# Kernel tuning notes

Measured on AMD Instinct MI355X. Metric: run time of the kernel, lower is better.

## Reference

```python
import jax, jax.numpy as jnp
import numpy as np

D_MODEL = 1024
N_HEAD = 16
DK = D_MODEL // N_HEAD
NEG = -10000.0  # module uses masked_fill with -10000.0, not -inf


def setup_inputs() -> dict:
    key = jax.random.key(0)
    k1, k2, k3 = jax.random.split(key, 3)
    B, T = 8, 1024
    x = jax.random.normal(k1, (B, T, D_MODEL), dtype=jnp.float32)
    # torch Linear(d, 3d, bias=False): y = x @ W.T with W [3d, d]; store transposed
    w_qkv = jax.random.normal(k2, (D_MODEL, 3 * D_MODEL), dtype=jnp.float32) * (1.0 / np.sqrt(D_MODEL))
    w_proj = jax.random.normal(k3, (D_MODEL, D_MODEL), dtype=jnp.float32) * (1.0 / np.sqrt(D_MODEL))
    return {"x": x, "w_qkv": w_qkv, "w_proj": w_proj}


def reference(x, w_qkv, w_proj):
    B, T, C = x.shape
    qkv = x @ w_qkv  # [B, T, 3C]
    q, k, v = jnp.split(qkv, 3, axis=-1)
    # [B, H, T, dk]
    q = q.reshape(B, T, N_HEAD, DK).transpose(0, 2, 1, 3)
    k = k.reshape(B, T, N_HEAD, DK).transpose(0, 2, 1, 3)
    v = v.reshape(B, T, N_HEAD, DK).transpose(0, 2, 1, 3)
    att = jnp.einsum('bhqd,bhkd->bhqk', q, k) / jnp.sqrt(jnp.float32(DK))
    causal = jnp.tril(jnp.ones((T, T), dtype=bool))  # [T, T]
    att = jnp.where(causal[None, None], att, NEG)
    att = jax.nn.softmax(att, axis=-1)
    y = jnp.einsum('bhqk,bhkd->bhqd', att, v)  # [B, H, T, dk]
    y = y.transpose(0, 2, 1, 3).reshape(B, T, C)
    return y @ w_proj
```

## Files before the change

kernel.cpp:

```cpp
#include <hip/hip_runtime.h>

typedef short bf16x8 __attribute__((ext_vector_type(8)));
typedef float f32x4 __attribute__((ext_vector_type(4)));

__device__ __forceinline__ unsigned short f2bf(float f) {
  unsigned u = __builtin_bit_cast(unsigned, f);
  u += 0x7fff + ((u >> 16) & 1);
  return (unsigned short)(u >> 16);
}

__device__ __forceinline__ void gload_lds16(const void* g, void* l) {
  __builtin_amdgcn_global_load_lds(
      (const __attribute__((address_space(1))) void*)g,
      (__attribute__((address_space(3))) void*)l, 16, 0, 0);
}

__global__ __launch_bounds__(256) void cvt_f32_bf16(const float* __restrict__ in,
                                                    unsigned short* __restrict__ out,
                                                    int n4) {
  int i = blockIdx.x * blockDim.x + threadIdx.x;
  int stride = gridDim.x * blockDim.x;
  for (; i < n4; i += stride) {
    float4 v = ((const float4*)in)[i];
    ushort4 o;
    o.x = f2bf(v.x); o.y = f2bf(v.y); o.z = f2bf(v.z); o.w = f2bf(v.w);
    ((ushort4*)out)[i] = o;
  }
}

__global__ __launch_bounds__(256) void tconv(const float* __restrict__ in,
                                             unsigned short* __restrict__ out,
                                             int R, int C) {
  __shared__ float tile[32][33];
  const int c0 = blockIdx.x * 32, r0 = blockIdx.y * 32;
  const int tid = threadIdx.x;
  const int tr = tid >> 3;
  const int tc4 = tid & 7;
  float4 v = *(const float4*)&in[(size_t)(r0 + tr) * C + c0 + tc4 * 4];
  tile[tr][tc4 * 4 + 0] = v.x;
  tile[tr][tc4 * 4 + 1] = v.y;
  tile[tr][tc4 * 4 + 2] = v.z;
  tile[tr][tc4 * 4 + 3] = v.w;
  __syncthreads();
#pragma unroll
  for (int i = 0; i < 4; ++i)
    out[(size_t)(c0 + tr) * R + r0 + tc4 * 4 + i] = f2bf(tile[tc4 * 4 + i][tr]);
}

__global__ __launch_bounds__(256) void transpV(const unsigned short* __restrict__ qkv,
                                               unsigned short* __restrict__ vT) {
  const int tt = blockIdx.x, bh = blockIdx.y;
  const int b = bh >> 4, h = bh & 15;
  __shared__ unsigned short tile[64 * 64];
  const int tid = threadIdx.x;
  const size_t gbase = (size_t)b * 1024 * 3072 + 2048 + (size_t)h * 64;
#pragma unroll
  for (int i = 0; i < 2; ++i) {
    int c = i * 256 + tid;
    int trow = c >> 3, dc = c & 7;
    *(uint4*)(&tile[c * 8]) =
        *(const uint4*)(qkv + gbase + (size_t)(tt * 64 + trow) * 3072 + dc * 8);
  }
  __syncthreads();
  const int d = tid & 63, th = tid >> 6;
  unsigned short buf[16];
#pragma unroll
  for (int j = 0; j < 16; ++j) buf[j] = tile[(th * 16 + j) * 64 + d];
  size_t obase = ((size_t)bh * 64 + d) * 1024 + tt * 64 + th * 16;
  *(uint4*)(&vT[obase]) = *(uint4*)(&buf[0]);
  *(uint4*)(&vT[obase + 8]) = *(uint4*)(&buf[8]);
}

template <int OUT_BF16>
__global__ __launch_bounds__(256) void gemm_bt(const unsigned short* __restrict__ A,
                                               const unsigned short* __restrict__ B,
                                               void* __restrict__ Cv,
                                               int M, int N, int K, int lda) {
  __shared__ unsigned short As[128 * 64];
  __shared__ unsigned short Bs[128 * 64];
  const int tid = threadIdx.x;
  const int wv = tid >> 6, lane = tid & 63;
  const int l15 = lane & 15, lg = lane >> 4;
  const int bm = blockIdx.y, bn = blockIdx.x;
  const int wr = wv >> 1, wc = wv & 1;
  f32x4 acc[4][4] = {};
  const unsigned short* Ab = A + (size_t)bm * 128 * lda;
  const unsigned short* Bb = B + (size_t)bn * 128 * K;

  for (int k0 = 0; k0 < K; k0 += 64) {
#pragma unroll
    for (int i = 0; i < 4; ++i) {
      int s = i * 256 + wv * 64 + lane;
      int row = s >> 3, pc = s & 7;
      int lc = pc ^ (row & 7);
      gload_lds16(Ab + (size_t)row * lda + k0 + lc * 8,
                  (char*)As + (size_t)(i * 256 + wv * 64) * 16);
      gload_lds16(Bb + (size_t)row * K + k0 + lc * 8,
                  (char*)Bs + (size_t)(i * 256 + wv * 64) * 16);
    }
    __syncthreads();
#pragma unroll
    for (int kh = 0; kh < 2; ++kh) {
      bf16x8 af[4], bf[4];
#pragma unroll
      for (int m = 0; m < 4; ++m) {
        int row = wr * 64 + m * 16 + l15;
        int pc = (kh * 4 + lg) ^ (row & 7);
        af[m] = *(const bf16x8*)((const char*)As + (row * 8 + pc) * 16);
      }
#pragma unroll
      for (int n = 0; n < 4; ++n) {
        int row = wc * 64 + n * 16 + l15;
        int pc = (kh * 4 + lg) ^ (row & 7);
        bf[n] = *(const bf16x8*)((const char*)Bs + (row * 8 + pc) * 16);
      }
#pragma unroll
      for (int m = 0; m < 4; ++m)
#pragma unroll
        for (int n = 0; n < 4; ++n)
          acc[m][n] = __builtin_amdgcn_mfma_f32_16x16x32_bf16(af[m], bf[n], acc[m][n], 0, 0, 0);
    }
    __syncthreads();
  }

  const int rbase = bm * 128 + wr * 64;
  const int cbase = bn * 128 + wc * 64;
#pragma unroll
  for (int m = 0; m < 4; ++m)
#pragma unroll
    for (int n = 0; n < 4; ++n)
#pragma unroll
      for (int r = 0; r < 4; ++r) {
        int row = rbase + m * 16 + lg * 4 + r;
        int col = cbase + n * 16 + l15;
        float v = acc[m][n][r];
        if (OUT_BF16)
          ((unsigned short*)Cv)[(size_t)row * N + col] = f2bf(v);
        else
          ((float*)Cv)[(size_t)row * N + col] = v;
      }
}

__global__ __launch_bounds__(256) void attn_fwd(const unsigned short* __restrict__ qkv,
                                                const unsigned short* __restrict__ vT,
                                                unsigned short* __restrict__ qkv_y) {
  const int pair = blockIdx.x;
  const int bh = blockIdx.y;
  const int b = bh >> 4, h = bh & 15;
  const int tid = threadIdx.x;
  const int wv = tid >> 6, lane = tid & 63;
  const int l15 = lane & 15, lg = lane >> 4;

  __shared__ unsigned short Ks[2][64 * 64];
  __shared__ unsigned short Vs[2][64 * 64];
  __shared__ unsigned short Ps[4][16][72];

  const size_t base = (size_t)b * 1024 * 3072;
  const float CSCL = 0.18033688f;

#pragma unroll
  for (int phase = 0; phase < 2; ++phase) {
    const int qt = phase ? 15 - pair : pair;
    const int q0 = qt * 64;
    const int qrow = q0 + wv * 16 + l15;
    const int rowg_base = q0 + wv * 16 + lg * 4;

    bf16x8 qa[2];
#pragma unroll
    for (int kh = 0; kh < 2; ++kh)
      qa[kh] = *(const bf16x8*)(qkv + base + (size_t)qrow * 3072 + h * 64 + kh * 32 + lg * 8);

    float l_r[4] = {0.f, 0.f, 0.f, 0.f};
    f32x4 oacc[4] = {};

#pragma unroll
    for (int i = 0; i < 2; ++i) {
      int s = i * 256 + wv * 64 + lane;
      int row = s >> 3, pc = s & 7;
      int lc = pc ^ (row & 7);
      gload_lds16(qkv + base + (size_t)row * 3072 + 1024 + h * 64 + lc * 8,
                  (char*)(&Ks[0][0]) + (size_t)s * 16);
      gload_lds16(vT + ((size_t)bh * 64 + row) * 1024 + lc * 8,
                  (char*)(&Vs[0][0]) + (size_t)s * 16);
    }
    __syncthreads();

    for (int t = 0; t <= qt; ++t) {
      const int cur = t & 1;
      if (t < qt) {
        const int kv1 = (t + 1) * 64;
#pragma unroll
        for (int i = 0; i < 2; ++i) {
          int s = i * 256 + wv * 64 + lane;
          int row = s >> 3, pc = s & 7;
          int lc = pc ^ (row & 7);
          gload_lds16(qkv + base + (size_t)(kv1 + row) * 3072 + 1024 + h * 64 + lc * 8,
                      (char*)(&Ks[cur ^ 1][0]) + (size_t)s * 16);
          gload_lds16(vT + ((size_t)bh * 64 + row) * 1024 + kv1 + lc * 8,
                      (char*)(&Vs[cur ^ 1][0]) + (size_t)s * 16);
        }
      }

      const int kv0 = t * 64;
      f32x4 sacc[4] = {};
#pragma unroll
      for (int kh = 0; kh < 2; ++kh) {
        bf16x8 kf[4];
#pragma unroll
        for (int nt = 0; nt < 4; ++nt) {
          int row = nt * 16 + l15;
          int pc = (kh * 4 + lg) ^ (row & 7);
          kf[nt] = *(const bf16x8*)((const char*)(&Ks[cur][0]) + (row * 8 + pc) * 16);
        }
#pragma unroll
        for (int nt = 0; nt < 4; ++nt)
          sacc[nt] = __builtin_amdgcn_mfma_f32_16x16x32_bf16(qa[kh], kf[nt], sacc[nt], 0, 0, 0);
      }

      const bool diag = (t == qt);
      float sv[4][4];
#pragma unroll
      for (int nt = 0; nt < 4; ++nt)
#pragma unroll
        for (int r = 0; r < 4; ++r) {
          float s = sacc[nt][r] * CSCL;
          if (diag && (kv0 + nt * 16 + l15 > rowg_base + r)) s = -1e30f;
          sv[nt][r] = exp2f(s);
        }

#pragma unroll
      for (int r = 0; r < 4; ++r) {
        float ps = (sv[0][r] + sv[1][r]) + (sv[2][r] + sv[3][r]);
        ps += __shfl_xor(ps, 1);
        ps += __shfl_xor(ps, 2);
        ps += __shfl_xor(ps, 4);
        ps += __shfl_xor(ps, 8);
        l_r[r] += ps;
      }

#pragma unroll
      for (int nt = 0; nt < 4; ++nt)
#pragma unroll
        for (int r = 0; r < 4; ++r)
          Ps[wv][lg * 4 + r][nt * 16 + l15] = f2bf(sv[nt][r]);

      bf16x8 pa[2];
#pragma unroll
      for (int kh = 0; kh < 2; ++kh)
        pa[kh] = *(const bf16x8*)&Ps[wv][l15][kh * 32 + lg * 8];

#pragma unroll
      for (int kh = 0; kh < 2; ++kh)
#pragma unroll
        for (int nt = 0; nt < 4; ++nt) {
          int row = nt * 16 + l15;
          int pc = (kh * 4 + lg) ^ (row & 7);
          bf16x8 vf = *(const bf16x8*)((const char*)(&Vs[cur][0]) + (row * 8 + pc) * 16);
          oacc[nt] = __builtin_amdgcn_mfma_f32_16x16x32_bf16(pa[kh], vf, oacc[nt], 0, 0, 0);
        }
      __syncthreads();
    }

#pragma unroll
    for (int nt = 0; nt < 4; ++nt) {
#pragma unroll
      for (int r = 0; r < 4; ++r) {
        int row = rowg_base + r;
        int col = h * 64 + nt * 16 + l15;
        qkv_y[((size_t)b * 1024 + row) * 3072 + 2048 + col] = f2bf(oacc[nt][r] / l_r[r]);
      }
    }
    __syncthreads();
  }
}

extern "C" void kernel_launch(void* const* d_in, const int* in_sizes, int n_in,
                              void* d_out, int out_size, void* d_ws, size_t ws_size,
                              hipStream_t stream) {
  const float* x = (const float*)d_in[0];
  const float* w_qkv = (const float*)d_in[1];
  const float* w_proj = (const float*)d_in[2];

  unsigned short* xb     = (unsigned short*)d_ws;
  unsigned short* vT     = (unsigned short*)d_ws;
  unsigned short* wqkvT  = (unsigned short*)((char*)d_ws + (16u << 20));
  unsigned short* wprojT = (unsigned short*)((char*)d_ws + (22u << 20));
  unsigned short* qkvb   = (unsigned short*)((char*)d_ws + (24u << 20));

  cvt_f32_bf16<<<2048, 256, 0, stream>>>(x, xb, (8 * 1024 * 1024) / 4);
  tconv<<<dim3(96, 32), 256, 0, stream>>>(w_qkv, wqkvT, 1024, 3072);
  tconv<<<dim3(32, 32), 256, 0, stream>>>(w_proj, wprojT, 1024, 1024);

  gemm_bt<1><<<dim3(24, 64), 256, 0, stream>>>(xb, wqkvT, qkvb, 8192, 3072, 1024, 1024);

  transpV<<<dim3(16, 128), 256, 0, stream>>>(qkvb, vT);

  attn_fwd<<<dim3(8, 128), 256, 0, stream>>>(qkvb, vT, qkvb);

  gemm_bt<0><<<dim3(8, 64), 256, 0, stream>>>(qkvb + 2048, wprojT, d_out, 8192, 1024, 1024, 3072);
}
```

Measured before the change: 265.2 us.

## Merge prep kernels, swap attention MFMA operands, pass P through registers via bpermute

Folds the three preprocessing launches (x conversion and two weight transposes) into one prep kernel to remove launch overhead. In attention, the QK^T MFMA now runs with swapped operands so each lane holds a column of S^T. That lets the row-sum reduction use two cross-lane shuffles, and the P tile is packed with v_cvt_pk_bf16_f32 and moved into A-operand layout with ds_bpermute instead of a round trip through shared memory. The attention grid is also reordered so that bh varies fastest. The costs are more bpermute traffic and a more intricate lane mapping that must match the MFMA layout exactly.

```diff
diff --git a/kernel.cpp b/kernel.cpp
--- a/kernel.cpp
+++ b/kernel.cpp
@@ -2,6 +2,7 @@
 
 typedef short bf16x8 __attribute__((ext_vector_type(8)));
 typedef float f32x4 __attribute__((ext_vector_type(4)));
+typedef unsigned u32x4 __attribute__((ext_vector_type(4)));
 
 __device__ __forceinline__ unsigned short f2bf(float f) {
   unsigned u = __builtin_bit_cast(unsigned, f);
@@ -15,25 +16,38 @@
       (__attribute__((address_space(3))) void*)l, 16, 0, 0);
 }
 
-__global__ __launch_bounds__(256) void cvt_f32_bf16(const float* __restrict__ in,
-                                                    unsigned short* __restrict__ out,
-                                                    int n4) {
-  int i = blockIdx.x * blockDim.x + threadIdx.x;
-  int stride = gridDim.x * blockDim.x;
-  for (; i < n4; i += stride) {
-    float4 v = ((const float4*)in)[i];
-    ushort4 o;
-    o.x = f2bf(v.x); o.y = f2bf(v.y); o.z = f2bf(v.z); o.w = f2bf(v.w);
-    ((ushort4*)out)[i] = o;
-  }
-}
-
-__global__ __launch_bounds__(256) void tconv(const float* __restrict__ in,
-                                             unsigned short* __restrict__ out,
-                                             int R, int C) {
+__global__ __launch_bounds__(256) void prep(const float* __restrict__ x,
+                                            const float* __restrict__ wqkv,
+                                            const float* __restrict__ wproj,
+                                            unsigned short* __restrict__ xb,
+                                            unsigned short* __restrict__ wqkvT,
+                                            unsigned short* __restrict__ wprojT) {
   __shared__ float tile[32][33];
-  const int c0 = blockIdx.x * 32, r0 = blockIdx.y * 32;
   const int tid = threadIdx.x;
+  const int bid = blockIdx.x;
+  if (bid < 2048) {
+    int i = bid * 256 + tid;
+    const int stride = 2048 * 256;
+    for (; i < 2097152; i += stride) {
+      float4 v = ((const float4*)x)[i];
+      ushort4 o;
+      o.x = f2bf(v.x); o.y = f2bf(v.y); o.z = f2bf(v.z); o.w = f2bf(v.w);
+      ((ushort4*)xb)[i] = o;
+    }
+    return;
+  }
+  const float* in;
+  unsigned short* out;
+  int R, C, c0, r0;
+  if (bid < 5120) {
+    int b = bid - 2048;
+    in = wqkv; out = wqkvT; R = 1024; C = 3072;
+    c0 = (b % 96) * 32; r0 = (b / 96) * 32;
+  } else {
+    int b = bid - 5120;
+    in = wproj; out = wprojT; R = 1024; C = 1024;
+    c0 = (b % 32) * 32; r0 = (b / 32) * 32;
+  }
   const int tr = tid >> 3;
   const int tc4 = tid & 7;
   float4 v = *(const float4*)&in[(size_t)(r0 + tr) * C + c0 + tc4 * 4];
@@ -144,8 +158,8 @@
 __global__ __launch_bounds__(256) void attn_fwd(const unsigned short* __restrict__ qkv,
                                                 const unsigned short* __restrict__ vT,
                                                 unsigned short* __restrict__ qkv_y) {
-  const int pair = blockIdx.x;
-  const int bh = blockIdx.y;
+  const int bh = blockIdx.x;
+  const int pair = blockIdx.y;
   const int b = bh >> 4, h = bh & 15;
   const int tid = threadIdx.x;
   const int wv = tid >> 6, lane = tid & 63;
@@ -153,10 +167,14 @@
 
   __shared__ unsigned short Ks[2][64 * 64];
   __shared__ unsigned short Vs[2][64 * 64];
-  __shared__ unsigned short Ps[4][16][72];
 
   const size_t base = (size_t)b * 1024 * 3072;
   const float CSCL = 0.18033688f;
+  const int kq = wv * 16 + l15;
+
+  const int idx0 = (l15 + ((lg & 1) << 5)) << 2;
+  const int idx1 = idx0 + 64;
+  const bool hi_nt = (lg & 2) != 0;
 
 #pragma unroll
   for (int phase = 0; phase < 2; ++phase) {
@@ -170,7 +188,7 @@
     for (int kh = 0; kh < 2; ++kh)
       qa[kh] = *(const bf16x8*)(qkv + base + (size_t)qrow * 3072 + h * 64 + kh * 32 + lg * 8);
 
-    float l_r[4] = {0.f, 0.f, 0.f, 0.f};
+    float l_sum = 0.f;
     f32x4 oacc[4] = {};
 
 #pragma unroll
@@ -201,7 +219,6 @@
         }
       }
 
-      const int kv0 = t * 64;
       f32x4 sacc[4] = {};
 #pragma unroll
       for (int kh = 0; kh < 2; ++kh) {
@@ -214,7 +231,7 @@
         }
 #pragma unroll
         for (int nt = 0; nt < 4; ++nt)
-          sacc[nt] = __builtin_amdgcn_mfma_f32_16x16x32_bf16(qa[kh], kf[nt], sacc[nt], 0, 0, 0);
+          sacc[nt] = __builtin_amdgcn_mfma_f32_16x16x32_bf16(kf[nt], qa[kh], sacc[nt], 0, 0, 0);
       }
 
       const bool diag = (t == qt);
@@ -224,30 +241,44 @@
 #pragma unroll
         for (int r = 0; r < 4; ++r) {
           float s = sacc[nt][r] * CSCL;
-          if (diag && (kv0 + nt * 16 + l15 > rowg_base + r)) s = -1e30f;
+          if (diag && (nt * 16 + lg * 4 + r > kq)) s = -1e30f;
           sv[nt][r] = exp2f(s);
         }
 
-#pragma unroll
-      for (int r = 0; r < 4; ++r) {
-        float ps = (sv[0][r] + sv[1][r]) + (sv[2][r] + sv[3][r]);
-        ps += __shfl_xor(ps, 1);
-        ps += __shfl_xor(ps, 2);
-        ps += __shfl_xor(ps, 4);
-        ps += __shfl_xor(ps, 8);
-        l_r[r] += ps;
-      }
-
+      {
+        float ts = 0.f;
+#pragma unroll
+        for (int nt = 0; nt < 4; ++nt)
+#pragma unroll
+          for (int r = 0; r < 4; ++r) ts += sv[nt][r];
+        ts += __shfl_xor(ts, 16);
+        ts += __shfl_xor(ts, 32);
+        l_sum += ts;
+      }
+
+      unsigned P2[4][2];
 #pragma unroll
       for (int nt = 0; nt < 4; ++nt)
 #pragma unroll
-        for (int r = 0; r < 4; ++r)
-          Ps[wv][lg * 4 + r][nt * 16 + l15] = f2bf(sv[nt][r]);
-
+        for (int i = 0; i < 2; ++i)
+          asm("v_cvt_pk_bf16_f32 %0, %1, %2"
+              : "=v"(P2[nt][i]) : "v"(sv[nt][2 * i]), "v"(sv[nt][2 * i + 1]));
+
+      u32x4 paw0, paw1;
+#pragma unroll
+      for (int w = 0; w < 4; ++w) {
+        int idx = (w & 2) ? idx1 : idx0;
+        int ri = w & 1;
+        unsigned a0 = (unsigned)__builtin_amdgcn_ds_bpermute(idx, (int)P2[0][ri]);
+        unsigned b0 = (unsigned)__builtin_amdgcn_ds_bpermute(idx, (int)P2[1][ri]);
+        paw0[w] = hi_nt ? b0 : a0;
+        unsigned a1 = (unsigned)__builtin_amdgcn_ds_bpermute(idx, (int)P2[2][ri]);
+        unsigned b1 = (unsigned)__builtin_amdgcn_ds_bpermute(idx, (int)P2[3][ri]);
+        paw1[w] = hi_nt ? b1 : a1;
+      }
       bf16x8 pa[2];
-#pragma unroll
-      for (int kh = 0; kh < 2; ++kh)
-        pa[kh] = *(const bf16x8*)&Ps[wv][l15][kh * 32 + lg * 8];
+      pa[0] = __builtin_bit_cast(bf16x8, paw0);
+      pa[1] = __builtin_bit_cast(bf16x8, paw1);
 
 #pragma unroll
       for (int kh = 0; kh < 2; ++kh)
@@ -261,13 +292,22 @@
       __syncthreads();
     }
 
+    float linv[4];
+#pragma unroll
+    for (int r = 0; r < 4; ++r) {
+      int q = lg * 4 + r;
+      float lv = __builtin_bit_cast(
+          float, __builtin_amdgcn_ds_bpermute(q << 2, __builtin_bit_cast(int, l_sum)));
+      linv[r] = 1.0f / lv;
+    }
+
 #pragma unroll
     for (int nt = 0; nt < 4; ++nt) {
 #pragma unroll
       for (int r = 0; r < 4; ++r) {
         int row = rowg_base + r;
         int col = h * 64 + nt * 16 + l15;
-        qkv_y[((size_t)b * 1024 + row) * 3072 + 2048 + col] = f2bf(oacc[nt][r] / l_r[r]);
+        qkv_y[((size_t)b * 1024 + row) * 3072 + 2048 + col] = f2bf(oacc[nt][r] * linv[r]);
       }
     }
     __syncthreads();
@@ -287,15 +327,13 @@
   unsigned short* wprojT = (unsigned short*)((char*)d_ws + (22u << 20));
   unsigned short* qkvb   = (unsigned short*)((char*)d_ws + (24u << 20));
 
-  cvt_f32_bf16<<<2048, 256, 0, stream>>>(x, xb, (8 * 1024 * 1024) / 4);
-  tconv<<<dim3(96, 32), 256, 0, stream>>>(w_qkv, wqkvT, 1024, 3072);
-  tconv<<<dim3(32, 32), 256, 0, stream>>>(w_proj, wprojT, 1024, 1024);
+  prep<<<6144, 256, 0, stream>>>(x, w_qkv, w_proj, xb, wqkvT, wprojT);
 
   gemm_bt<1><<<dim3(24, 64), 256, 0, stream>>>(xb, wqkvT, qkvb, 8192, 3072, 1024, 1024);
 
   transpV<<<dim3(16, 128), 256, 0, stream>>>(qkvb, vT);
 
-  attn_fwd<<<dim3(8, 128), 256, 0, stream>>>(qkvb, vT, qkvb);
+  attn_fwd<<<dim3(128, 8), 256, 0, stream>>>(qkvb, vT, qkvb);
 
   gemm_bt<0><<<dim3(8, 64), 256, 0, stream>>>(qkvb + 2048, wprojT, d_out, 8192, 1024, 1024, 3072);
 }
```

Result: faster. 230.3 us (-13.2%).
